# Optimization experiments

Measured on AMD Instinct MI355X. Metric: run time of the kernel, lower is better.

Reference implementation:

```python
import jax, jax.numpy as jnp
import numpy as np
import math

S, B, D = 1024, 8, 512
H = 8
HD = D // H
DFF = 2048
NUM_BUCKETS = 32
MAX_DISTANCE = 128
LN_EPS = 1e-5


def setup_inputs() -> dict:
    key = jax.random.key(0)
    ks = jax.random.split(key, 12)
    s = 0.02
    return {
        "x": jax.random.normal(ks[0], (S, B, D), jnp.float32),
        "attn_mask": jnp.zeros((S, S), jnp.float32),
        "in_proj_w": jax.random.normal(ks[1], (3 * D, D), jnp.float32) * s,
        "in_proj_b": jnp.zeros((3 * D,), jnp.float32),
        "out_proj_w": jax.random.normal(ks[2], (D, D), jnp.float32) * s,
        "out_proj_b": jnp.zeros((D,), jnp.float32),
        "lin1_w": jax.random.normal(ks[3], (DFF, D), jnp.float32) * s,
        "lin1_b": jnp.zeros((DFF,), jnp.float32),
        "lin2_w": jax.random.normal(ks[4], (D, DFF), jnp.float32) * s,
        "lin2_b": jnp.zeros((D,), jnp.float32),
        "ln1_w": jnp.ones((D,), jnp.float32),
        "ln1_b": jnp.zeros((D,), jnp.float32),
        "ln2_w": jnp.ones((D,), jnp.float32),
        "ln2_b": jnp.zeros((D,), jnp.float32),
        "rel_emb": jax.random.normal(ks[5], (NUM_BUCKETS, H), jnp.float32) * s,
    }


def _relative_position_bucket(relative_position, num_buckets=NUM_BUCKETS, max_distance=MAX_DISTANCE):
    # bidirectional=True path (encoder)
    nb = num_buckets // 2
    rel_buckets = (relative_position > 0).astype(jnp.int32) * nb
    rp = jnp.abs(relative_position)
    max_exact = nb // 2
    is_small = rp < max_exact
    rp_safe = jnp.maximum(rp, 1)  # avoid log(0); masked by is_small below
    rp_large = max_exact + (
        jnp.log(rp_safe.astype(jnp.float32) / max_exact)
        / math.log(max_distance / max_exact)
        * (nb - max_exact)
    ).astype(jnp.int32)
    rp_large = jnp.minimum(rp_large, nb - 1)
    return rel_buckets + jnp.where(is_small, rp, rp_large)


def _compute_bias(rel_emb, q_len, k_len):
    ctx = jnp.arange(q_len, dtype=jnp.int32)[:, None]
    mem = jnp.arange(k_len, dtype=jnp.int32)[None, :]
    buckets = _relative_position_bucket(mem - ctx)          # [S, S]
    values = rel_emb[buckets]                                # [S, S, H]
    return jnp.transpose(values, (2, 0, 1))                  # [H, S, S]


def _layer_norm(x, w, b):
    mu = jnp.mean(x, axis=-1, keepdims=True)
    var = jnp.mean(jnp.square(x - mu), axis=-1, keepdims=True)
    return (x - mu) * jax.lax.rsqrt(var + LN_EPS) * w + b


def reference(x, attn_mask, in_proj_w, in_proj_b, out_proj_w, out_proj_b,
              lin1_w, lin1_b, lin2_w, lin2_b, ln1_w, ln1_b, ln2_w, ln2_b, rel_emb):
    s, b, d = x.shape
    # qkv projection (torch Linear: y = x W^T + b)
    qkv = x @ in_proj_w.T + in_proj_b                         # [S, B, 3D]
    q, k, v = jnp.split(qkv, 3, axis=-1)

    def to_bhsd(t):
        return jnp.transpose(t.reshape(s, b, H, HD), (1, 2, 0, 3))  # [B, H, S, HD]

    q, k, v = to_bhsd(q), to_bhsd(k), to_bhsd(v)
    scores = jnp.einsum("bhqd,bhkd->bhqk", q, k) / math.sqrt(HD)

    bias = _compute_bias(rel_emb, s, s)                       # [H, S, S]
    mask_bias = attn_mask[None, :, :] + bias                  # [H, S, S]
    attn = jax.nn.softmax(scores + mask_bias[None], axis=-1)  # [B, H, S, S]

    o = jnp.einsum("bhqk,bhkd->bhqd", attn, v)                # [B, H, S, HD]
    o = jnp.transpose(o, (2, 0, 1, 3)).reshape(s, b, d)       # [S, B, D]
    o = o @ out_proj_w.T + out_proj_b

    # post-norm (norm_first=False)
    y = _layer_norm(x + o, ln1_w, ln1_b)
    ff = jax.nn.relu(y @ lin1_w.T + lin1_b) @ lin2_w.T + lin2_b
    return _layer_norm(y + ff, ln2_w, ln2_b)
```

## Files before the change

### kernel.cpp

```cpp
#include <hip/hip_runtime.h>
#include <hip/hip_bf16.h>


#define S_LEN 1024
#define BATCH 8
#define DMODEL 512
#define NHEAD 8
#define HDIM 64
#define DFF 2048
#define NROWS (S_LEN * BATCH)

typedef __bf16 bf16x8 __attribute__((ext_vector_type(8)));
typedef short  s16x4  __attribute__((ext_vector_type(4)));
typedef float  f32x4  __attribute__((ext_vector_type(4)));

__device__ __forceinline__ void gload16(const void* g, void* l) {
    __builtin_amdgcn_global_load_lds(
        (const __attribute__((address_space(1))) void*)g,
        (__attribute__((address_space(3))) void*)l, 16, 0, 0);
}

__global__ __launch_bounds__(256)
void prep_kernel(const float* __restrict__ x,
                 const float* __restrict__ wq, const float* __restrict__ wo,
                 const float* __restrict__ w1, const float* __restrict__ w2,
                 __hip_bfloat16* __restrict__ xb, __hip_bfloat16* __restrict__ wqb,
                 __hip_bfloat16* __restrict__ wob, __hip_bfloat16* __restrict__ w1b,
                 __hip_bfloat16* __restrict__ w2b) {
    const int NX = NROWS * DMODEL / 4;
    const int NQ = 3 * DMODEL * DMODEL / 4;
    const int NO = DMODEL * DMODEL / 4;
    const int N1 = DFF * DMODEL / 4;
    int i = blockIdx.x * 256 + threadIdx.x;
    const float* src; __hip_bfloat16* dst; int off;
    if (i < NX)                         { src = x;  dst = xb;  off = i; }
    else if ((i -= NX) < NQ)            { src = wq; dst = wqb; off = i; }
    else if ((i -= NQ) < NO)            { src = wo; dst = wob; off = i; }
    else if ((i -= NO) < N1)            { src = w1; dst = w1b; off = i; }
    else if ((i -= N1) < N1)            { src = w2; dst = w2b; off = i; }
    else return;
    float4 v = *(const float4*)(src + (size_t)off * 4);
    union { s16x4 s; __hip_bfloat16 b[4]; } u;
    u.b[0] = __float2bfloat16(v.x); u.b[1] = __float2bfloat16(v.y);
    u.b[2] = __float2bfloat16(v.z); u.b[3] = __float2bfloat16(v.w);
    *(s16x4*)(dst + (size_t)off * 4) = u.s;
}

__global__ __launch_bounds__(256)
void embc_kernel(const float* __restrict__ mask,
                 const float* __restrict__ rel_emb,
                 __hip_bfloat16* __restrict__ embC) {
    int tid = blockIdx.x * 256 + threadIdx.x;
    int h  = tid >> 16;
    int r1 = tid & 65535;
    int qt = r1 >> 12;
    int w  = (r1 >> 10) & 3;
    int kb = (r1 >> 6) & 15;
    int lane = r1 & 63;
    int q = qt * 64 + w * 16 + (lane & 15);
    __hip_bfloat16 ov[16];
#pragma unroll
    for (int j = 0; j < 16; ++j) {
        int c = j >> 2, e = j & 3;
        int k = kb * 64 + c * 16 + (lane >> 4) * 4 + e;
        int rel = k - q;
        int bucket = (rel > 0) ? 16 : 0;
        int rp = rel < 0 ? -rel : rel;
        int v;
        if (rp < 8)          v = rp;
        else if (rp < 12)    v = 8;
        else if (rp < 16)    v = 9;
        else if (rp < 23)    v = 10;
        else if (rp < 32)    v = 11;
        else if (rp < 46)    v = 12;
        else if (rp < 64)    v = 13;
        else if (rp < 91)    v = 14;
        else                 v = 15;
        float bt = rel_emb[(bucket + v) * NHEAD + h];
        ov[j] = __float2bfloat16(__expf(mask[(size_t)q * S_LEN + k] + bt));
    }
    *(uint4*)(embC + (size_t)tid * 16) = *(uint4*)&ov[0];
    *(uint4*)(embC + (size_t)tid * 16 + 8) = *(uint4*)&ov[8];
}

template <int MODE, bool RELU>
__global__ __launch_bounds__(256)
void gemm_tile(const __hip_bfloat16* __restrict__ Ab,
               const __hip_bfloat16* __restrict__ Wb,
               const float* __restrict__ bias,
               void* __restrict__ outv,
               int N, int M, int K) {
    const int w = threadIdx.x >> 6;
    const int lane = threadIdx.x & 63;
    const int m16 = lane & 15;
    const int quad = lane >> 4;
    const int row0 = blockIdx.y * 128;
    const int col0 = blockIdx.x * 128;
    const int rowbase = (w >> 1) * 64;
    const int colbase = (w & 1) * 64;

    __shared__ __align__(16) __bf16 As[128 * 64];
    __shared__ __align__(16) __bf16 Bs[128 * 64];

    const __bf16* Ap = (const __bf16*)Ab;
    const __bf16* Wp = (const __bf16*)Wb;

    const int a_row_in_grp = lane >> 3;
    const int kb_sw = (lane & 7) ^ (lane >> 3);

    f32x4 acc[4][4];
#pragma unroll
    for (int c = 0; c < 4; ++c)
#pragma unroll
        for (int r = 0; r < 4; ++r) acc[c][r] = f32x4{0, 0, 0, 0};

    for (int k0 = 0; k0 < K; k0 += 64) {
#pragma unroll
        for (int i = 0; i < 4; ++i) {
            int grp = w * 4 + i;
            int row = grp * 8 + a_row_in_grp;
            gload16(Ap + (size_t)(row0 + row) * K + k0 + kb_sw * 8,
                    (void*)(As + grp * 512));
            gload16(Wp + (size_t)(col0 + row) * K + k0 + kb_sw * 8,
                    (void*)(Bs + grp * 512));
        }
        __syncthreads();

#pragma unroll
        for (int kk = 0; kk < 2; ++kk) {
            bf16x8 af[4], bfr[4];
            int slot = (kk * 4 + quad) ^ (m16 & 7);
#pragma unroll
            for (int r = 0; r < 4; ++r)
                af[r] = *(const bf16x8*)(As + (rowbase + r * 16 + m16) * 64 + slot * 8);
#pragma unroll
            for (int c = 0; c < 4; ++c)
                bfr[c] = *(const bf16x8*)(Bs + (colbase + c * 16 + m16) * 64 + slot * 8);
#pragma unroll
            for (int c = 0; c < 4; ++c)
#pragma unroll
                for (int r = 0; r < 4; ++r)
                    acc[c][r] = __builtin_amdgcn_mfma_f32_16x16x32_bf16(
                        af[r], bfr[c], acc[c][r], 0, 0, 0);
        }
        __syncthreads();
    }

#pragma unroll
    for (int c = 0; c < 4; ++c) {
        int col = col0 + colbase + c * 16 + m16;
        float bv = bias[col];
#pragma unroll
        for (int r = 0; r < 4; ++r) {
#pragma unroll
            for (int e = 0; e < 4; ++e) {
                int row = row0 + rowbase + r * 16 + quad * 4 + e;
                float v = acc[c][r][e] + bv;
                if (RELU) v = fmaxf(v, 0.f);
                if (MODE == 1) {
                    ((__hip_bfloat16*)outv)[(size_t)row * M + col] = __float2bfloat16(v);
                } else {
                    int sect = col >> 9, h = (col >> 6) & 7, d = col & 63;
                    int s = row >> 3, bb = row & 7;
                    size_t idx;
                    if (sect == 2)
                        idx = (size_t)(128 + bb * 8 + h) * (S_LEN * HDIM)
                            + (size_t)d * S_LEN + s;
                    else
                        idx = ((size_t)(sect * 64 + bb * 8 + h) * S_LEN + s) * HDIM + d;
                    ((__hip_bfloat16*)outv)[idx] = __float2bfloat16(v);
                }
            }
        }
    }
}

__global__ __launch_bounds__(256)
void gemm64_db(const __hip_bfloat16* __restrict__ Ab,
               const __hip_bfloat16* __restrict__ Wb,
               const float* __restrict__ bias,
               float* __restrict__ outf,
               int N, int M, int K) {
    const int w = threadIdx.x >> 6;
    const int lane = threadIdx.x & 63;
    const int m16 = lane & 15;
    const int quad = lane >> 4;
    const int row0 = blockIdx.y * 128;
    const int col0 = blockIdx.x * 64;
    const int rowbase = w * 32;

    __shared__ __align__(16) __bf16 As[2][128 * 64];
    __shared__ __align__(16) __bf16 Bs[2][64 * 64];

    const __bf16* Ap = (const __bf16*)Ab;
    const __bf16* Wp = (const __bf16*)Wb;

    const int a_row_in_grp = lane >> 3;
    const int kb_sw = (lane & 7) ^ (lane >> 3);

    auto stage = [&](int k0, int p) {
#pragma unroll
        for (int i = 0; i < 4; ++i) {
            int grp = w * 4 + i;
            int row = grp * 8 + a_row_in_grp;
            gload16(Ap + (size_t)(row0 + row) * K + k0 + kb_sw * 8,
                    (void*)(&As[p][grp * 512]));
        }
#pragma unroll
        for (int i = 0; i < 2; ++i) {
            int grp = w * 2 + i;
            int row = grp * 8 + a_row_in_grp;
            gload16(Wp + (size_t)(col0 + row) * K + k0 + kb_sw * 8,
                    (void*)(&Bs[p][grp * 512]));
        }
    };

    f32x4 acc[4][2];
#pragma unroll
    for (int c = 0; c < 4; ++c)
#pragma unroll
        for (int r = 0; r < 2; ++r) acc[c][r] = f32x4{0, 0, 0, 0};

    stage(0, 0);
    __syncthreads();

    int p = 0;
    for (int k0 = 0; k0 < K; k0 += 64, p ^= 1) {
        if (k0 + 64 < K) stage(k0 + 64, p ^ 1);
#pragma unroll
        for (int kk = 0; kk < 2; ++kk) {
            bf16x8 af[2], bfr[4];
            int slot = (kk * 4 + quad) ^ (m16 & 7);
#pragma unroll
            for (int r = 0; r < 2; ++r)
                af[r] = *(const bf16x8*)(&As[p][(rowbase + r * 16 + m16) * 64 + slot * 8]);
#pragma unroll
            for (int c = 0; c < 4; ++c)
                bfr[c] = *(const bf16x8*)(&Bs[p][(c * 16 + m16) * 64 + slot * 8]);
#pragma unroll
            for (int c = 0; c < 4; ++c)
#pragma unroll
                for (int r = 0; r < 2; ++r)
                    acc[c][r] = __builtin_amdgcn_mfma_f32_16x16x32_bf16(
                        af[r], bfr[c], acc[c][r], 0, 0, 0);
        }
        __syncthreads();
    }

#pragma unroll
    for (int c = 0; c < 4; ++c) {
        int col = col0 + c * 16 + m16;
        float bv = bias[col];
#pragma unroll
        for (int r = 0; r < 2; ++r)
#pragma unroll
            for (int e = 0; e < 4; ++e) {
                int row = row0 + rowbase + r * 16 + quad * 4 + e;
                outf[(size_t)row * M + col] = acc[c][r][e] + bv;
            }
    }
}

__global__ __launch_bounds__(256, 4)
void attn_mfma(const __hip_bfloat16* __restrict__ qkv_bhsd,
               const __hip_bfloat16* __restrict__ embC,
               __hip_bfloat16* __restrict__ o) {
    const int bh = blockIdx.y;
    const int b = bh >> 3, h = bh & 7;
    const int qt = blockIdx.x;
    const int q0 = qt * 64;
    const int t = threadIdx.x;
    const int w = t >> 6, lane = t & 63, m16 = lane & 15, quad = lane >> 4;

    const __bf16* Qb  = (const __bf16*)qkv_bhsd + (size_t)bh * (S_LEN * HDIM);
    const __bf16* Kb  = (const __bf16*)qkv_bhsd + (size_t)(64 + bh) * (S_LEN * HDIM);
    const __bf16* VTg = (const __bf16*)qkv_bhsd + (size_t)(128 + bh) * (S_LEN * HDIM);
    const __hip_bfloat16* ec =
        embC + ((((size_t)h * 16 + qt) * 4 + w) * 16) * 1024 + (size_t)lane * 16;

    __shared__ __align__(16) __bf16 Ks[2][64 * 64];
    __shared__ __align__(16) __bf16 Vs[2][64 * 64];
    __shared__ __align__(16) __bf16 P[4][16 * 64];

    const int r_in = lane >> 3;
    const int kb_sw = (lane & 7) ^ r_in;

    auto stage = [&](int kc, int p) {
#pragma unroll
        for (int i = 0; i < 2; ++i) {
            int grp = w * 2 + i;
            gload16(Kb + (size_t)(kc + grp * 8 + r_in) * HDIM + kb_sw * 8,
                    (void*)(&Ks[p][grp * 512]));
            gload16(VTg + (size_t)(grp * 8 + r_in) * S_LEN + kc + kb_sw * 8,
                    (void*)(&Vs[p][grp * 512]));
        }
    };

    bf16x8 aQ0, aQ1;
    {
        const __bf16* qp = Qb + (size_t)(q0 + w * 16 + m16) * HDIM + quad * 8;
        bf16x8 t0 = *(const bf16x8*)qp;
        bf16x8 t1 = *(const bf16x8*)(qp + 32);
#pragma unroll
        for (int j = 0; j < 8; ++j) {
            t0[j] = (__bf16)((float)t0[j] * 0.125f);
            t1[j] = (__bf16)((float)t1[j] * 0.125f);
        }
        aQ0 = t0; aQ1 = t1;
    }

    f32x4 accOT[4] = {f32x4{0,0,0,0}, f32x4{0,0,0,0}, f32x4{0,0,0,0}, f32x4{0,0,0,0}};
    float lpart = 0.f;

    stage(0, 0);
    __syncthreads();

    int p = 0;
    for (int kc = 0; kc < S_LEN; kc += 64, p ^= 1) {
        if (kc + 64 < S_LEN) stage(kc + 64, p ^ 1);

        union { uint4 u[2]; __hip_bfloat16 e[16]; } ev;
        ev.u[0] = *(const uint4*)(ec + (size_t)(kc >> 6) * 1024);
        ev.u[1] = *(const uint4*)(ec + (size_t)(kc >> 6) * 1024 + 8);

        f32x4 accT[4] = {f32x4{0,0,0,0}, f32x4{0,0,0,0}, f32x4{0,0,0,0}, f32x4{0,0,0,0}};
        const int sub = (m16 >> 3) * 512 + (m16 & 7) * 64;
        const int s0 = (quad ^ (m16 & 7)) * 8;
        const int s1 = ((4 + quad) ^ (m16 & 7)) * 8;
#pragma unroll
        for (int c = 0; c < 4; ++c) {
            const __bf16* kr = &Ks[p][c * 1024 + sub];
            bf16x8 b0 = *(const bf16x8*)(kr + s0);
            bf16x8 b1 = *(const bf16x8*)(kr + s1);
            accT[c] = __builtin_amdgcn_mfma_f32_16x16x32_bf16(b0, aQ0, accT[c], 0, 0, 0);
            accT[c] = __builtin_amdgcn_mfma_f32_16x16x32_bf16(b1, aQ1, accT[c], 0, 0, 0);
        }

#pragma unroll
        for (int c = 0; c < 4; ++c) {
            union { s16x4 s; __hip_bfloat16 bb[4]; } u;
#pragma unroll
            for (int e = 0; e < 4; ++e) {
                float pv = __expf(accT[c][e]) * __bfloat162float(ev.e[c * 4 + e]);
                lpart += pv;
                u.bb[e] = __float2bfloat16(pv);
            }
            int blk = (c * 2 + (quad >> 1)) ^ (m16 & 7);
            *(s16x4*)&P[w][m16 * 64 + blk * 8 + (quad & 1) * 4] = u.s;
        }

        bf16x8 pb0 = *(const bf16x8*)&P[w][m16 * 64 + ((quad) ^ (m16 & 7)) * 8];
        bf16x8 pb1 = *(const bf16x8*)&P[w][m16 * 64 + ((4 + quad) ^ (m16 & 7)) * 8];

#pragma unroll
        for (int dt = 0; dt < 4; ++dt) {
            const __bf16* vr = &Vs[p][dt * 1024 + sub];
            bf16x8 v0 = *(const bf16x8*)(vr + s0);
            bf16x8 v1 = *(const bf16x8*)(vr + s1);
            accOT[dt] = __builtin_amdgcn_mfma_f32_16x16x32_bf16(v0, pb0, accOT[dt], 0, 0, 0);
            accOT[dt] = __builtin_amdgcn_mfma_f32_16x16x32_bf16(v1, pb1, accOT[dt], 0, 0, 0);
        }

        __syncthreads();
    }

    float l = lpart;
    l += __shfl_xor(l, 16);
    l += __shfl_xor(l, 32);
    float inv = 1.f / l;

    {
        int q = q0 + w * 16 + m16;
        __hip_bfloat16* op = o + ((size_t)q * BATCH + b) * DMODEL + h * HDIM;
#pragma unroll
        for (int dt = 0; dt < 4; ++dt) {
            union { s16x4 s; __hip_bfloat16 bb[4]; } u;
#pragma unroll
            for (int e = 0; e < 4; ++e)
                u.bb[e] = __float2bfloat16(accOT[dt][e] * inv);
            *(s16x4*)(op + dt * 16 + quad * 4) = u.s;
        }
    }
}

__global__ __launch_bounds__(64)
void ln_kernel(const float* __restrict__ resid,
               const float* __restrict__ gin,
               const float* __restrict__ w,
               const float* __restrict__ b,
               float* __restrict__ outf,
               __hip_bfloat16* __restrict__ outb) {
    const int row = blockIdx.x;
    const int lane = threadIdx.x;
    const float* rp = resid + (size_t)row * DMODEL;
    const float* gp = gin + (size_t)row * DMODEL;

    float v[8];
    float s = 0.f, s2 = 0.f;
#pragma unroll
    for (int i = 0; i < 8; ++i) {
        int d = i * 64 + lane;
        float x = rp[d] + gp[d];
        v[i] = x;
        s += x;
        s2 += x * x;
    }
#pragma unroll
    for (int off = 32; off; off >>= 1) {
        s  += __shfl_xor(s, off);
        s2 += __shfl_xor(s2, off);
    }
    float mu = s * (1.f / DMODEL);
    float var = s2 * (1.f / DMODEL) - mu * mu;
    float rs = rsqrtf(var + 1e-5f);
#pragma unroll
    for (int i = 0; i < 8; ++i) {
        int d = i * 64 + lane;
        float y = (v[i] - mu) * rs * w[d] + b[d];
        outf[(size_t)row * DMODEL + d] = y;
        if (outb) outb[(size_t)row * DMODEL + d] = __float2bfloat16(y);
    }
}

extern "C" void kernel_launch(void* const* d_in, const int* in_sizes, int n_in,
                              void* d_out, int out_size, void* d_ws, size_t ws_size,
                              hipStream_t stream) {
    const float* x          = (const float*)d_in[0];
    const float* attn_mask  = (const float*)d_in[1];
    const float* in_proj_w  = (const float*)d_in[2];
    const float* in_proj_b  = (const float*)d_in[3];
    const float* out_proj_w = (const float*)d_in[4];
    const float* out_proj_b = (const float*)d_in[5];
    const float* lin1_w     = (const float*)d_in[6];
    const float* lin1_b     = (const float*)d_in[7];
    const float* lin2_w     = (const float*)d_in[8];
    const float* lin2_b     = (const float*)d_in[9];
    const float* ln1_w      = (const float*)d_in[10];
    const float* ln1_b      = (const float*)d_in[11];
    const float* ln2_w      = (const float*)d_in[12];
    const float* ln2_b      = (const float*)d_in[13];
    const float* rel_emb    = (const float*)d_in[14];

    char* ws = (char*)d_ws;
    size_t off = 0;
    auto alloc = [&](size_t bytes) {
        char* p = ws + off;
        off += (bytes + 255) / 256 * 256;
        return (void*)p;
    };
    __hip_bfloat16* embt  = (__hip_bfloat16*)alloc((size_t)NHEAD * S_LEN * S_LEN * 2);
    __hip_bfloat16* wqkvb = (__hip_bfloat16*)alloc((size_t)3 * DMODEL * DMODEL * 2);
    __hip_bfloat16* wob   = (__hip_bfloat16*)alloc((size_t)DMODEL * DMODEL * 2);
    __hip_bfloat16* w1b   = (__hip_bfloat16*)alloc((size_t)DFF * DMODEL * 2);
    __hip_bfloat16* w2b   = (__hip_bfloat16*)alloc((size_t)DMODEL * DFF * 2);
    __hip_bfloat16* xb    = (__hip_bfloat16*)alloc((size_t)NROWS * DMODEL * 2);
    __hip_bfloat16* qkvb  = (__hip_bfloat16*)alloc((size_t)3 * 64 * S_LEN * HDIM * 2);
    __hip_bfloat16* o     = (__hip_bfloat16*)alloc((size_t)NROWS * DMODEL * 2);
    float* tmp            = (float*)alloc((size_t)NROWS * DMODEL * 4);
    float* yf             = (float*)alloc((size_t)NROWS * DMODEL * 4);
    __hip_bfloat16* yb    = (__hip_bfloat16*)alloc((size_t)NROWS * DMODEL * 2);
    __hip_bfloat16* ffb   = (__hip_bfloat16*)alloc((size_t)NROWS * DFF * 2);

    float* out = (float*)d_out;

    prep_kernel<<<dim3(7168), 256, 0, stream>>>(
        x, in_proj_w, out_proj_w, lin1_w, lin2_w, xb, wqkvb, wob, w1b, w2b);
    embc_kernel<<<dim3(2048), 256, 0, stream>>>(attn_mask, rel_emb, embt);

    gemm_tile<2, false><<<dim3(12, 64), 256, 0, stream>>>(
        xb, wqkvb, in_proj_b, qkvb, NROWS, 3 * DMODEL, DMODEL);

    attn_mfma<<<dim3(S_LEN / 64, BATCH * NHEAD), 256, 0, stream>>>(
        qkvb, embt, o);

    gemm64_db<<<dim3(8, 64), 256, 0, stream>>>(
        o, wob, out_proj_b, tmp, NROWS, DMODEL, DMODEL);

    ln_kernel<<<dim3(NROWS), 64, 0, stream>>>(x, tmp, ln1_w, ln1_b, yf, yb);

    gemm_tile<1, true><<<dim3(16, 64), 256, 0, stream>>>(
        yb, w1b, lin1_b, ffb, NROWS, DFF, DMODEL);

    gemm64_db<<<dim3(8, 64), 256, 0, stream>>>(
        ffb, w2b, lin2_b, tmp, NROWS, DMODEL, DFF);

    ln_kernel<<<dim3(NROWS), 64, 0, stream>>>(yf, tmp, ln2_w, ln2_b, out, nullptr);
}
```

Before: 292.4 us.

## Fuse prep kernels, widen attention q-tile, split-K the FFN2 GEMM

```diff
diff --git a/kernel.cpp b/kernel.cpp
--- a/kernel.cpp
+++ b/kernel.cpp
@@ -21,66 +21,66 @@
 }
 
 __global__ __launch_bounds__(256)
-void prep_kernel(const float* __restrict__ x,
-                 const float* __restrict__ wq, const float* __restrict__ wo,
-                 const float* __restrict__ w1, const float* __restrict__ w2,
-                 __hip_bfloat16* __restrict__ xb, __hip_bfloat16* __restrict__ wqb,
-                 __hip_bfloat16* __restrict__ wob, __hip_bfloat16* __restrict__ w1b,
-                 __hip_bfloat16* __restrict__ w2b) {
-    const int NX = NROWS * DMODEL / 4;
-    const int NQ = 3 * DMODEL * DMODEL / 4;
-    const int NO = DMODEL * DMODEL / 4;
-    const int N1 = DFF * DMODEL / 4;
-    int i = blockIdx.x * 256 + threadIdx.x;
-    const float* src; __hip_bfloat16* dst; int off;
-    if (i < NX)                         { src = x;  dst = xb;  off = i; }
-    else if ((i -= NX) < NQ)            { src = wq; dst = wqb; off = i; }
-    else if ((i -= NQ) < NO)            { src = wo; dst = wob; off = i; }
-    else if ((i -= NO) < N1)            { src = w1; dst = w1b; off = i; }
-    else if ((i -= N1) < N1)            { src = w2; dst = w2b; off = i; }
-    else return;
-    float4 v = *(const float4*)(src + (size_t)off * 4);
-    union { s16x4 s; __hip_bfloat16 b[4]; } u;
-    u.b[0] = __float2bfloat16(v.x); u.b[1] = __float2bfloat16(v.y);
-    u.b[2] = __float2bfloat16(v.z); u.b[3] = __float2bfloat16(v.w);
-    *(s16x4*)(dst + (size_t)off * 4) = u.s;
-}
-
-__global__ __launch_bounds__(256)
-void embc_kernel(const float* __restrict__ mask,
-                 const float* __restrict__ rel_emb,
-                 __hip_bfloat16* __restrict__ embC) {
-    int tid = blockIdx.x * 256 + threadIdx.x;
-    int h  = tid >> 16;
-    int r1 = tid & 65535;
-    int qt = r1 >> 12;
-    int w  = (r1 >> 10) & 3;
-    int kb = (r1 >> 6) & 15;
-    int lane = r1 & 63;
-    int q = qt * 64 + w * 16 + (lane & 15);
-    __hip_bfloat16 ov[16];
-#pragma unroll
-    for (int j = 0; j < 16; ++j) {
-        int c = j >> 2, e = j & 3;
-        int k = kb * 64 + c * 16 + (lane >> 4) * 4 + e;
-        int rel = k - q;
-        int bucket = (rel > 0) ? 16 : 0;
-        int rp = rel < 0 ? -rel : rel;
-        int v;
-        if (rp < 8)          v = rp;
-        else if (rp < 12)    v = 8;
-        else if (rp < 16)    v = 9;
-        else if (rp < 23)    v = 10;
-        else if (rp < 32)    v = 11;
-        else if (rp < 46)    v = 12;
-        else if (rp < 64)    v = 13;
-        else if (rp < 91)    v = 14;
-        else                 v = 15;
-        float bt = rel_emb[(bucket + v) * NHEAD + h];
-        ov[j] = __float2bfloat16(__expf(mask[(size_t)q * S_LEN + k] + bt));
-    }
-    *(uint4*)(embC + (size_t)tid * 16) = *(uint4*)&ov[0];
-    *(uint4*)(embC + (size_t)tid * 16 + 8) = *(uint4*)&ov[8];
+void prep_embc_kernel(const float* __restrict__ x,
+                      const float* __restrict__ wq, const float* __restrict__ wo,
+                      const float* __restrict__ w1, const float* __restrict__ w2,
+                      __hip_bfloat16* __restrict__ xb, __hip_bfloat16* __restrict__ wqb,
+                      __hip_bfloat16* __restrict__ wob, __hip_bfloat16* __restrict__ w1b,
+                      __hip_bfloat16* __restrict__ w2b,
+                      const float* __restrict__ mask,
+                      const float* __restrict__ rel_emb,
+                      __hip_bfloat16* __restrict__ embC) {
+    if (blockIdx.x < 7168) {
+        const int NX = NROWS * DMODEL / 4;
+        const int NQ = 3 * DMODEL * DMODEL / 4;
+        const int NO = DMODEL * DMODEL / 4;
+        const int N1 = DFF * DMODEL / 4;
+        int i = blockIdx.x * 256 + threadIdx.x;
+        const float* src; __hip_bfloat16* dst; int off;
+        if (i < NX)                         { src = x;  dst = xb;  off = i; }
+        else if ((i -= NX) < NQ)            { src = wq; dst = wqb; off = i; }
+        else if ((i -= NQ) < NO)            { src = wo; dst = wob; off = i; }
+        else if ((i -= NO) < N1)            { src = w1; dst = w1b; off = i; }
+        else if ((i -= N1) < N1)            { src = w2; dst = w2b; off = i; }
+        else return;
+        float4 v = *(const float4*)(src + (size_t)off * 4);
+        union { s16x4 s; __hip_bfloat16 b[4]; } u;
+        u.b[0] = __float2bfloat16(v.x); u.b[1] = __float2bfloat16(v.y);
+        u.b[2] = __float2bfloat16(v.z); u.b[3] = __float2bfloat16(v.w);
+        *(s16x4*)(dst + (size_t)off * 4) = u.s;
+    } else {
+        int tid = (blockIdx.x - 7168) * 256 + threadIdx.x;
+        int h  = tid >> 16;
+        int r1 = tid & 65535;
+        int qt = r1 >> 12;
+        int w  = (r1 >> 10) & 3;
+        int kb = (r1 >> 6) & 15;
+        int lane = r1 & 63;
+        int q = qt * 64 + w * 16 + (lane & 15);
+        __hip_bfloat16 ov[16];
+#pragma unroll
+        for (int j = 0; j < 16; ++j) {
+            int c = j >> 2, e = j & 3;
+            int k = kb * 64 + c * 16 + (lane >> 4) * 4 + e;
+            int rel = k - q;
+            int bucket = (rel > 0) ? 16 : 0;
+            int rp = rel < 0 ? -rel : rel;
+            int v;
+            if (rp < 8)          v = rp;
+            else if (rp < 12)    v = 8;
+            else if (rp < 16)    v = 9;
+            else if (rp < 23)    v = 10;
+            else if (rp < 32)    v = 11;
+            else if (rp < 46)    v = 12;
+            else if (rp < 64)    v = 13;
+            else if (rp < 91)    v = 14;
+            else                 v = 15;
+            float bt = rel_emb[(bucket + v) * NHEAD + h];
+            ov[j] = __float2bfloat16(__expf(mask[(size_t)q * S_LEN + k] + bt));
+        }
+        *(uint4*)(embC + (size_t)tid * 16) = *(uint4*)&ov[0];
+        *(uint4*)(embC + (size_t)tid * 16 + 8) = *(uint4*)&ov[8];
+    }
 }
 
 template <int MODE, bool RELU>
@@ -89,13 +89,14 @@
                const __hip_bfloat16* __restrict__ Wb,
                const float* __restrict__ bias,
                void* __restrict__ outv,
-               int N, int M, int K) {
+               int N, int M, int Kloop, int Kstride) {
     const int w = threadIdx.x >> 6;
     const int lane = threadIdx.x & 63;
     const int m16 = lane & 15;
     const int quad = lane >> 4;
     const int row0 = blockIdx.y * 128;
     const int col0 = blockIdx.x * 128;
+    const int kbase = blockIdx.z * Kloop;
     const int rowbase = (w >> 1) * 64;
     const int colbase = (w & 1) * 64;
 
@@ -114,14 +115,14 @@
 #pragma unroll
         for (int r = 0; r < 4; ++r) acc[c][r] = f32x4{0, 0, 0, 0};
 
-    for (int k0 = 0; k0 < K; k0 += 64) {
+    for (int k0 = 0; k0 < Kloop; k0 += 64) {
 #pragma unroll
         for (int i = 0; i < 4; ++i) {
             int grp = w * 4 + i;
             int row = grp * 8 + a_row_in_grp;
-            gload16(Ap + (size_t)(row0 + row) * K + k0 + kb_sw * 8,
+            gload16(Ap + (size_t)(row0 + row) * Kstride + kbase + k0 + kb_sw * 8,
                     (void*)(As + grp * 512));
-            gload16(Wp + (size_t)(col0 + row) * K + k0 + kb_sw * 8,
+            gload16(Wp + (size_t)(col0 + row) * Kstride + kbase + k0 + kb_sw * 8,
                     (void*)(Bs + grp * 512));
         }
         __syncthreads();
@@ -149,7 +150,7 @@
 #pragma unroll
     for (int c = 0; c < 4; ++c) {
         int col = col0 + colbase + c * 16 + m16;
-        float bv = bias[col];
+        float bv = (MODE == 0 && blockIdx.z != 0) ? 0.f : bias[col];
 #pragma unroll
         for (int r = 0; r < 4; ++r) {
 #pragma unroll
@@ -157,7 +158,9 @@
                 int row = row0 + rowbase + r * 16 + quad * 4 + e;
                 float v = acc[c][r][e] + bv;
                 if (RELU) v = fmaxf(v, 0.f);
-                if (MODE == 1) {
+                if (MODE == 0) {
+                    ((float*)outv)[(size_t)blockIdx.z * N * M + (size_t)row * M + col] = v;
+                } else if (MODE == 1) {
                     ((__hip_bfloat16*)outv)[(size_t)row * M + col] = __float2bfloat16(v);
                 } else {
                     int sect = col >> 9, h = (col >> 6) & 7, d = col & 63;
@@ -261,26 +264,28 @@
     }
 }
 
-__global__ __launch_bounds__(256, 4)
+__global__ __launch_bounds__(256, 2)
 void attn_mfma(const __hip_bfloat16* __restrict__ qkv_bhsd,
                const __hip_bfloat16* __restrict__ embC,
                __hip_bfloat16* __restrict__ o) {
     const int bh = blockIdx.y;
     const int b = bh >> 3, h = bh & 7;
-    const int qt = blockIdx.x;
-    const int q0 = qt * 64;
+    const int q0 = blockIdx.x * 128;
     const int t = threadIdx.x;
     const int w = t >> 6, lane = t & 63, m16 = lane & 15, quad = lane >> 4;
 
     const __bf16* Qb  = (const __bf16*)qkv_bhsd + (size_t)bh * (S_LEN * HDIM);
     const __bf16* Kb  = (const __bf16*)qkv_bhsd + (size_t)(64 + bh) * (S_LEN * HDIM);
     const __bf16* VTg = (const __bf16*)qkv_bhsd + (size_t)(128 + bh) * (S_LEN * HDIM);
-    const __hip_bfloat16* ec =
-        embC + ((((size_t)h * 16 + qt) * 4 + w) * 16) * 1024 + (size_t)lane * 16;
+    const int qtA = blockIdx.x * 2, qtB = qtA + 1;
+    const __hip_bfloat16* ecA =
+        embC + ((((size_t)h * 16 + qtA) * 4 + w) * 16) * 1024 + (size_t)lane * 16;
+    const __hip_bfloat16* ecB =
+        embC + ((((size_t)h * 16 + qtB) * 4 + w) * 16) * 1024 + (size_t)lane * 16;
 
     __shared__ __align__(16) __bf16 Ks[2][64 * 64];
     __shared__ __align__(16) __bf16 Vs[2][64 * 64];
-    __shared__ __align__(16) __bf16 P[4][16 * 64];
+    __shared__ __align__(16) __bf16 P[4][2][16 * 64];
 
     const int r_in = lane >> 3;
     const int kb_sw = (lane & 7) ^ r_in;
@@ -296,21 +301,27 @@
         }
     };
 
-    bf16x8 aQ0, aQ1;
+    bf16x8 aQ0A, aQ1A, aQ0B, aQ1B;
     {
-        const __bf16* qp = Qb + (size_t)(q0 + w * 16 + m16) * HDIM + quad * 8;
-        bf16x8 t0 = *(const bf16x8*)qp;
-        bf16x8 t1 = *(const bf16x8*)(qp + 32);
+        const __bf16* qpA = Qb + (size_t)(q0 + w * 16 + m16) * HDIM + quad * 8;
+        const __bf16* qpB = qpA + (size_t)64 * HDIM;
+        bf16x8 t0 = *(const bf16x8*)qpA;
+        bf16x8 t1 = *(const bf16x8*)(qpA + 32);
+        bf16x8 t2 = *(const bf16x8*)qpB;
+        bf16x8 t3 = *(const bf16x8*)(qpB + 32);
 #pragma unroll
         for (int j = 0; j < 8; ++j) {
             t0[j] = (__bf16)((float)t0[j] * 0.125f);
             t1[j] = (__bf16)((float)t1[j] * 0.125f);
-        }
-        aQ0 = t0; aQ1 = t1;
-    }
-
-    f32x4 accOT[4] = {f32x4{0,0,0,0}, f32x4{0,0,0,0}, f32x4{0,0,0,0}, f32x4{0,0,0,0}};
-    float lpart = 0.f;
+            t2[j] = (__bf16)((float)t2[j] * 0.125f);
+            t3[j] = (__bf16)((float)t3[j] * 0.125f);
+        }
+        aQ0A = t0; aQ1A = t1; aQ0B = t2; aQ1B = t3;
+    }
+
+    f32x4 accOTA[4] = {f32x4{0,0,0,0}, f32x4{0,0,0,0}, f32x4{0,0,0,0}, f32x4{0,0,0,0}};
+    f32x4 accOTB[4] = {f32x4{0,0,0,0}, f32x4{0,0,0,0}, f32x4{0,0,0,0}, f32x4{0,0,0,0}};
+    float lpartA = 0.f, lpartB = 0.f;
 
     stage(0, 0);
     __syncthreads();
@@ -319,11 +330,14 @@
     for (int kc = 0; kc < S_LEN; kc += 64, p ^= 1) {
         if (kc + 64 < S_LEN) stage(kc + 64, p ^ 1);
 
-        union { uint4 u[2]; __hip_bfloat16 e[16]; } ev;
-        ev.u[0] = *(const uint4*)(ec + (size_t)(kc >> 6) * 1024);
-        ev.u[1] = *(const uint4*)(ec + (size_t)(kc >> 6) * 1024 + 8);
-
-        f32x4 accT[4] = {f32x4{0,0,0,0}, f32x4{0,0,0,0}, f32x4{0,0,0,0}, f32x4{0,0,0,0}};
+        union { uint4 u[2]; __hip_bfloat16 e[16]; } evA, evB;
+        evA.u[0] = *(const uint4*)(ecA + (size_t)(kc >> 6) * 1024);
+        evA.u[1] = *(const uint4*)(ecA + (size_t)(kc >> 6) * 1024 + 8);
+        evB.u[0] = *(const uint4*)(ecB + (size_t)(kc >> 6) * 1024);
+        evB.u[1] = *(const uint4*)(ecB + (size_t)(kc >> 6) * 1024 + 8);
+
+        f32x4 accTA[4] = {f32x4{0,0,0,0}, f32x4{0,0,0,0}, f32x4{0,0,0,0}, f32x4{0,0,0,0}};
+        f32x4 accTB[4] = {f32x4{0,0,0,0}, f32x4{0,0,0,0}, f32x4{0,0,0,0}, f32x4{0,0,0,0}};
         const int sub = (m16 >> 3) * 512 + (m16 & 7) * 64;
         const int s0 = (quad ^ (m16 & 7)) * 8;
         const int s1 = ((4 + quad) ^ (m16 & 7)) * 8;
@@ -332,53 +346,66 @@
             const __bf16* kr = &Ks[p][c * 1024 + sub];
             bf16x8 b0 = *(const bf16x8*)(kr + s0);
             bf16x8 b1 = *(const bf16x8*)(kr + s1);
-            accT[c] = __builtin_amdgcn_mfma_f32_16x16x32_bf16(b0, aQ0, accT[c], 0, 0, 0);
-            accT[c] = __builtin_amdgcn_mfma_f32_16x16x32_bf16(b1, aQ1, accT[c], 0, 0, 0);
+            accTA[c] = __builtin_amdgcn_mfma_f32_16x16x32_bf16(b0, aQ0A, accTA[c], 0, 0, 0);
+            accTA[c] = __builtin_amdgcn_mfma_f32_16x16x32_bf16(b1, aQ1A, accTA[c], 0, 0, 0);
+            accTB[c] = __builtin_amdgcn_mfma_f32_16x16x32_bf16(b0, aQ0B, accTB[c], 0, 0, 0);
+            accTB[c] = __builtin_amdgcn_mfma_f32_16x16x32_bf16(b1, aQ1B, accTB[c], 0, 0, 0);
         }
 
 #pragma unroll
         for (int c = 0; c < 4; ++c) {
-            union { s16x4 s; __hip_bfloat16 bb[4]; } u;
+            union { s16x4 s; __hip_bfloat16 bb[4]; } uA, uB;
 #pragma unroll
             for (int e = 0; e < 4; ++e) {
-                float pv = __expf(accT[c][e]) * __bfloat162float(ev.e[c * 4 + e]);
-                lpart += pv;
-                u.bb[e] = __float2bfloat16(pv);
+                float pvA = __expf(accTA[c][e]) * __bfloat162float(evA.e[c * 4 + e]);
+                float pvB = __expf(accTB[c][e]) * __bfloat162float(evB.e[c * 4 + e]);
+                lpartA += pvA; lpartB += pvB;
+                uA.bb[e] = __float2bfloat16(pvA);
+                uB.bb[e] = __float2bfloat16(pvB);
             }
             int blk = (c * 2 + (quad >> 1)) ^ (m16 & 7);
-            *(s16x4*)&P[w][m16 * 64 + blk * 8 + (quad & 1) * 4] = u.s;
-        }
-
-        bf16x8 pb0 = *(const bf16x8*)&P[w][m16 * 64 + ((quad) ^ (m16 & 7)) * 8];
-        bf16x8 pb1 = *(const bf16x8*)&P[w][m16 * 64 + ((4 + quad) ^ (m16 & 7)) * 8];
+            *(s16x4*)&P[w][0][m16 * 64 + blk * 8 + (quad & 1) * 4] = uA.s;
+            *(s16x4*)&P[w][1][m16 * 64 + blk * 8 + (quad & 1) * 4] = uB.s;
+        }
+
+        bf16x8 pb0A = *(const bf16x8*)&P[w][0][m16 * 64 + ((quad) ^ (m16 & 7)) * 8];
+        bf16x8 pb1A = *(const bf16x8*)&P[w][0][m16 * 64 + ((4 + quad) ^ (m16 & 7)) * 8];
+        bf16x8 pb0B = *(const bf16x8*)&P[w][1][m16 * 64 + ((quad) ^ (m16 & 7)) * 8];
+        bf16x8 pb1B = *(const bf16x8*)&P[w][1][m16 * 64 + ((4 + quad) ^ (m16 & 7)) * 8];
 
 #pragma unroll
         for (int dt = 0; dt < 4; ++dt) {
             const __bf16* vr = &Vs[p][dt * 1024 + sub];
             bf16x8 v0 = *(const bf16x8*)(vr + s0);
             bf16x8 v1 = *(const bf16x8*)(vr + s1);
-            accOT[dt] = __builtin_amdgcn_mfma_f32_16x16x32_bf16(v0, pb0, accOT[dt], 0, 0, 0);
-            accOT[dt] = __builtin_amdgcn_mfma_f32_16x16x32_bf16(v1, pb1, accOT[dt], 0, 0, 0);
+            accOTA[dt] = __builtin_amdgcn_mfma_f32_16x16x32_bf16(v0, pb0A, accOTA[dt], 0, 0, 0);
+            accOTA[dt] = __builtin_amdgcn_mfma_f32_16x16x32_bf16(v1, pb1A, accOTA[dt], 0, 0, 0);
+            accOTB[dt] = __builtin_amdgcn_mfma_f32_16x16x32_bf16(v0, pb0B, accOTB[dt], 0, 0, 0);
+            accOTB[dt] = __builtin_amdgcn_mfma_f32_16x16x32_bf16(v1, pb1B, accOTB[dt], 0, 0, 0);
         }
 
         __syncthreads();
     }
 
-    float l = lpart;
-    l += __shfl_xor(l, 16);
-    l += __shfl_xor(l, 32);
-    float inv = 1.f / l;
+    float lA = lpartA, lB = lpartB;
+    lA += __shfl_xor(lA, 16); lA += __shfl_xor(lA, 32);
+    lB += __shfl_xor(lB, 16); lB += __shfl_xor(lB, 32);
+    float invA = 1.f / lA, invB = 1.f / lB;
 
     {
-        int q = q0 + w * 16 + m16;
-        __hip_bfloat16* op = o + ((size_t)q * BATCH + b) * DMODEL + h * HDIM;
+        int qA = q0 + w * 16 + m16;
+        __hip_bfloat16* opA = o + ((size_t)qA * BATCH + b) * DMODEL + h * HDIM;
+        __hip_bfloat16* opB = opA + (size_t)64 * BATCH * DMODEL;
 #pragma unroll
         for (int dt = 0; dt < 4; ++dt) {
-            union { s16x4 s; __hip_bfloat16 bb[4]; } u;
-#pragma unroll
-            for (int e = 0; e < 4; ++e)
-                u.bb[e] = __float2bfloat16(accOT[dt][e] * inv);
-            *(s16x4*)(op + dt * 16 + quad * 4) = u.s;
+            union { s16x4 s; __hip_bfloat16 bb[4]; } uA, uB;
+#pragma unroll
+            for (int e = 0; e < 4; ++e) {
+                uA.bb[e] = __float2bfloat16(accOTA[dt][e] * invA);
+                uB.bb[e] = __float2bfloat16(accOTB[dt][e] * invB);
+            }
+            *(s16x4*)(opA + dt * 16 + quad * 4) = uA.s;
+            *(s16x4*)(opB + dt * 16 + quad * 4) = uB.s;
         }
     }
 }
@@ -386,6 +413,7 @@
 __global__ __launch_bounds__(64)
 void ln_kernel(const float* __restrict__ resid,
                const float* __restrict__ gin,
+               const float* __restrict__ gin2,
                const float* __restrict__ w,
                const float* __restrict__ b,
                float* __restrict__ outf,
@@ -394,6 +422,7 @@
     const int lane = threadIdx.x;
     const float* rp = resid + (size_t)row * DMODEL;
     const float* gp = gin + (size_t)row * DMODEL;
+    const float* gp2 = gin2 ? gin2 + (size_t)row * DMODEL : nullptr;
 
     float v[8];
     float s = 0.f, s2 = 0.f;
@@ -401,6 +430,7 @@
     for (int i = 0; i < 8; ++i) {
         int d = i * 64 + lane;
         float x = rp[d] + gp[d];
+        if (gin2) x += gp2[d];
         v[i] = x;
         s += x;
         s2 += x * x;
@@ -456,33 +486,34 @@
     __hip_bfloat16* xb    = (__hip_bfloat16*)alloc((size_t)NROWS * DMODEL * 2);
     __hip_bfloat16* qkvb  = (__hip_bfloat16*)alloc((size_t)3 * 64 * S_LEN * HDIM * 2);
     __hip_bfloat16* o     = (__hip_bfloat16*)alloc((size_t)NROWS * DMODEL * 2);
-    float* tmp            = (float*)alloc((size_t)NROWS * DMODEL * 4);
+    float* tmp            = (float*)alloc((size_t)2 * NROWS * DMODEL * 4);
     float* yf             = (float*)alloc((size_t)NROWS * DMODEL * 4);
     __hip_bfloat16* yb    = (__hip_bfloat16*)alloc((size_t)NROWS * DMODEL * 2);
     __hip_bfloat16* ffb   = (__hip_bfloat16*)alloc((size_t)NROWS * DFF * 2);
 
     float* out = (float*)d_out;
-
-    prep_kernel<<<dim3(7168), 256, 0, stream>>>(
-        x, in_proj_w, out_proj_w, lin1_w, lin2_w, xb, wqkvb, wob, w1b, w2b);
-    embc_kernel<<<dim3(2048), 256, 0, stream>>>(attn_mask, rel_emb, embt);
+    float* tmp2 = tmp + (size_t)NROWS * DMODEL;
+
+    prep_embc_kernel<<<dim3(9216), 256, 0, stream>>>(
+        x, in_proj_w, out_proj_w, lin1_w, lin2_w, xb, wqkvb, wob, w1b, w2b,
+        attn_mask, rel_emb, embt);
 
     gemm_tile<2, false><<<dim3(12, 64), 256, 0, stream>>>(
-        xb, wqkvb, in_proj_b, qkvb, NROWS, 3 * DMODEL, DMODEL);
-
-    attn_mfma<<<dim3(S_LEN / 64, BATCH * NHEAD), 256, 0, stream>>>(
+        xb, wqkvb, in_proj_b, qkvb, NROWS, 3 * DMODEL, DMODEL, DMODEL);
+
+    attn_mfma<<<dim3(S_LEN / 128, BATCH * NHEAD), 256, 0, stream>>>(
         qkvb, embt, o);
 
     gemm64_db<<<dim3(8, 64), 256, 0, stream>>>(
         o, wob, out_proj_b, tmp, NROWS, DMODEL, DMODEL);
 
-    ln_kernel<<<dim3(NROWS), 64, 0, stream>>>(x, tmp, ln1_w, ln1_b, yf, yb);
+    ln_kernel<<<dim3(NROWS), 64, 0, stream>>>(x, tmp, nullptr, ln1_w, ln1_b, yf, yb);
 
     gemm_tile<1, true><<<dim3(16, 64), 256, 0, stream>>>(
-        yb, w1b, lin1_b, ffb, NROWS, DFF, DMODEL);
-
-    gemm64_db<<<dim3(8, 64), 256, 0, stream>>>(
-        ffb, w2b, lin2_b, tmp, NROWS, DMODEL, DFF);
-
-    ln_kernel<<<dim3(NROWS), 64, 0, stream>>>(yf, tmp, ln2_w, ln2_b, out, nullptr);
-}
+        yb, w1b, lin1_b, ffb, NROWS, DFF, DMODEL, DMODEL);
+
+    gemm_tile<0, false><<<dim3(4, 64, 2), 256, 0, stream>>>(
+        ffb, w2b, lin2_b, tmp, NROWS, DMODEL, DFF / 2, DFF);
+
+    ln_kernel<<<dim3(NROWS), 64, 0, stream>>>(yf, tmp, tmp2, ln2_w, ln2_b, out, nullptr);
+}
```

Measured after the change: 276.7 us. 1.06x faster.
